# Optimization experiments

Measured on AMD Instinct MI355X. Metric: run time of the kernel, lower is better.

## Reference

```python
import jax, jax.numpy as jnp
import numpy as np


def setup_inputs() -> dict:
    key = jax.random.key(0)
    ks = jax.random.split(key, 8)
    b, cin, cout, h, w, t, ssize = 4, 128, 128, 64, 64, 16, 512
    return {
        "x": jax.random.normal(ks[0], (b, cin, h, w, t), jnp.float32),
        "style": jax.random.normal(ks[1], (b, ssize), jnp.float32),
        "noise": jax.random.normal(ks[2], (b, 1, h, w, t), jnp.float32),
        # learned params
        "weight": jax.random.normal(ks[3], (cout, cin, 3, 3, 1), jnp.float32),
        "style_w": jax.random.normal(ks[4], (cin, ssize), jnp.float32) * 0.02,
        "style_b": jax.random.normal(ks[5], (cin,), jnp.float32) * 0.02,
        "noise_param": jax.random.normal(ks[6], (cout, 1, 1, 1), jnp.float32) * 0.1,
        "bias_param": jax.random.normal(ks[7], (cout, 1, 1, 1), jnp.float32) * 0.1,
    }


def reference(x, style, noise, weight, style_w, style_b, noise_param, bias_param):
    # style modulation scale per (batch, in-channel)
    s = style @ style_w.T + style_b                         # [b, cin]
    # Demodulation factor per (b, out). Mathematically identical to building
    # per-sample weights W[o,i,k]*s[b,i] and demodulating, but computed as a
    # tiny contraction instead of materializing [b,out,in,k,k,1] weights.
    sig_inv = jax.lax.rsqrt(
        jnp.einsum('oihwt,bi->bo', weight**2, s**2) + 1e-8)  # [b, cout]
    # Since conv is linear in its input, scaling input channels by s and the
    # output channels by sig_inv equals the grouped per-sample conv.
    x_mod = x * s[:, :, None, None, None]                   # [b, cin, h, w, t]
    y = jax.lax.conv_general_dilated(
        x_mod, weight, window_strides=(1, 1, 1), padding='SAME',
        dimension_numbers=('NCDHW', 'OIDHW', 'NCDHW'))      # [b, cout, h, w, t]
    y = y * sig_inv[:, :, None, None, None]
    # noise_param/bias_param are [cout,1,1,1]; broadcast over (h,w,t)
    return y + noise_param * noise + bias_param
```

## Files before the change

### kernel.cpp

```cpp
#include <hip/hip_runtime.h>
#include <hip/hip_bf16.h>
#include <stdint.h>

typedef __bf16 bf16;
typedef bf16 bf16x8 __attribute__((ext_vector_type(8)));
typedef float f32x4 __attribute__((ext_vector_type(4)));
typedef float f32x16 __attribute__((ext_vector_type(16)));


__global__ void k_style(const float* __restrict__ style, const float* __restrict__ sw,
                        const float* __restrict__ sbias, float* __restrict__ s_out) {
    int gw = (blockIdx.x * blockDim.x + threadIdx.x) >> 6;
    int lane = threadIdx.x & 63;
    if (gw >= 512) return;
    int b = gw >> 7, c = gw & 127;
    const float* st = style + b * 512;
    const float* wr = sw + c * 512;
    float a = 0.f;
#pragma unroll
    for (int j = 0; j < 8; ++j) a += st[lane + 64 * j] * wr[lane + 64 * j];
    for (int off = 32; off > 0; off >>= 1) a += __shfl_down(a, off, 64);
    if (lane == 0) s_out[gw] = a + sbias[c];
}

__global__ void k_sig(const float* __restrict__ weight, const float* __restrict__ s,
                      float* __restrict__ sig) {
    int gw = (blockIdx.x * blockDim.x + threadIdx.x) >> 6;
    int lane = threadIdx.x & 63;
    if (gw >= 512) return;
    int b = gw >> 7, o = gw & 127;
    float a = 0.f;
#pragma unroll
    for (int j = 0; j < 2; ++j) {
        int i = lane + 64 * j;
        const float* wr = weight + ((size_t)o * 128 + i) * 9;
        float wsq = 0.f;
#pragma unroll
        for (int t = 0; t < 9; ++t) wsq += wr[t] * wr[t];
        float sv = s[b * 128 + i];
        a += wsq * sv * sv;
    }
    for (int off = 32; off > 0; off >>= 1) a += __shfl_down(a, off, 64);
    if (lane == 0) sig[gw] = rsqrtf(a + 1e-8f);
}

__global__ void k_wt(const float* __restrict__ weight, const float* __restrict__ s,
                     bf16* __restrict__ wt) {
    int i = blockIdx.x * 256 + threadIdx.x;
    if (i >= 589824) return;
    int j = i & 7;
    int co = (i >> 3) & 127;
    int g = (i >> 10) & 1;
    int tap = (i >> 11) % 9;
    int cb = (i >> 11) / 9;
    int chunk = cb & 7, b = cb >> 3;
    int ci = chunk * 16 + g * 8 + j;
    wt[i] = (bf16)(weight[((size_t)co * 128 + ci) * 9 + tap] * s[b * 128 + ci]);
}

__global__ __launch_bounds__(256, 2) void conv_main(
    const float* __restrict__ x, const bf16* __restrict__ wt,
    const float* __restrict__ sig_inv, const float* __restrict__ npar,
    const float* __restrict__ bpar, const float* __restrict__ noise,
    float* __restrict__ out) {
    __shared__ bf16 Xl[2][1728 * 8];

    const int tid = threadIdx.x;
    const int lane = tid & 63;
    const int l31 = lane & 31, lhi = lane >> 5;
    const int wm = (tid >> 6) & 1;
    const int wn = tid >> 7;
    const int w0 = blockIdx.x * 16;
    const int h = blockIdx.y;
    const int b = blockIdx.z;
    const size_t bHW = (size_t)b * 65536;

    auto stage = [&](int chunk, bf16* buf) {
        const bf16 zz = (bf16)0.f;
        const bf16x8 vz = {zz, zz, zz, zz, zz, zz, zz, zz};
#pragma unroll
        for (int it = 0; it < 7; ++it) {
            int u = it * 256 + tid;
            if (u < 1728) {
                int dh = u / 576;
                int rem = u - dh * 576;
                int g = rem / 288;
                int e = rem - g * 288;
                int ha = h - 1 + dh;
                int wa = w0 - 1 + (e >> 4);
                bool ok = ((unsigned)ha < 64u) & ((unsigned)wa < 64u);
                int E = (ha * 64 + wa) * 16 + (e & 15);
                int Ec = ok ? E : 0;
                const float* xp =
                    x + (((size_t)(b * 128 + chunk * 16 + g * 8)) << 16) + Ec;
                bf16x8 v;
#pragma unroll
                for (int j = 0; j < 8; ++j) v[j] = (bf16)xp[(size_t)j << 16];
                v = ok ? v : vz;
                *(bf16x8*)&buf[u * 8] = v;
            }
        }
    };

    f32x16 acc[2][4] = {};

    const size_t ebase = bHW + (size_t)h * 1024 + w0 * 16 + wn * 128;
    float ns[4];
#pragma unroll
    for (int nf = 0; nf < 4; ++nf) ns[nf] = noise[ebase + nf * 32 + l31];

    stage(0, Xl[0]);

    for (int chunk = 0; chunk < 8; ++chunk) {
        __syncthreads();
        if (chunk < 7) stage(chunk + 1, Xl[(chunk + 1) & 1]);
        const bf16* Xb = Xl[chunk & 1];
        const bf16* wb = wt + (size_t)b * 147456;

#pragma unroll
        for (int tap = 0; tap < 9; ++tap) {
            const int dh = tap / 3, dw = tap % 3;
            const bf16* wg = wb +
                ((size_t)((chunk * 9 + tap) * 2 + lhi) * 128 + wm * 64 + l31) * 8;
            bf16x8 a0 = *(const bf16x8*)&wg[0];
            bf16x8 a1 = *(const bf16x8*)&wg[32 * 8];
            const bf16* xb = &Xb[((dh * 2 + lhi) * 288 + dw * 16 + wn * 128 + l31) * 8];
            bf16x8 b0 = *(const bf16x8*)&xb[0];
            bf16x8 b1 = *(const bf16x8*)&xb[32 * 8];
            bf16x8 b2 = *(const bf16x8*)&xb[64 * 8];
            bf16x8 b3 = *(const bf16x8*)&xb[96 * 8];
            acc[0][0] = __builtin_amdgcn_mfma_f32_32x32x16_bf16(a0, b0, acc[0][0], 0, 0, 0);
            acc[0][1] = __builtin_amdgcn_mfma_f32_32x32x16_bf16(a0, b1, acc[0][1], 0, 0, 0);
            acc[0][2] = __builtin_amdgcn_mfma_f32_32x32x16_bf16(a0, b2, acc[0][2], 0, 0, 0);
            acc[0][3] = __builtin_amdgcn_mfma_f32_32x32x16_bf16(a0, b3, acc[0][3], 0, 0, 0);
            acc[1][0] = __builtin_amdgcn_mfma_f32_32x32x16_bf16(a1, b0, acc[1][0], 0, 0, 0);
            acc[1][1] = __builtin_amdgcn_mfma_f32_32x32x16_bf16(a1, b1, acc[1][1], 0, 0, 0);
            acc[1][2] = __builtin_amdgcn_mfma_f32_32x32x16_bf16(a1, b2, acc[1][2], 0, 0, 0);
            acc[1][3] = __builtin_amdgcn_mfma_f32_32x32x16_bf16(a1, b3, acc[1][3], 0, 0, 0);
        }
    }

#pragma unroll
    for (int fm = 0; fm < 2; ++fm) {
        int cob = wm * 64 + fm * 32 + 4 * lhi;
#pragma unroll
        for (int q = 0; q < 4; ++q) {
            int co4 = cob + 8 * q;
            f32x4 sg = *(const f32x4*)&sig_inv[b * 128 + co4];
            f32x4 np4 = *(const f32x4*)&npar[co4];
            f32x4 bp4 = *(const f32x4*)&bpar[co4];
#pragma unroll
            for (int r = 0; r < 4; ++r) {
                int co = co4 + r;
                float* orow = out + ((size_t)(b * 128 + co) * 64 + h) * 1024 +
                              w0 * 16 + wn * 128;
#pragma unroll
                for (int nf = 0; nf < 4; ++nf) {
                    float v = acc[fm][nf][q * 4 + r];
                    orow[nf * 32 + l31] = v * sg[r] + np4[r] * ns[nf] + bp4[r];
                }
            }
        }
    }
}

__global__ void k_naive(const float* __restrict__ x, const float* __restrict__ weight,
                        const float* __restrict__ s, const float* __restrict__ sig,
                        const float* __restrict__ npar, const float* __restrict__ bpar,
                        const float* __restrict__ noise, float* __restrict__ out) {
    size_t o = (size_t)blockIdx.x * 256 + threadIdx.x;
    int t = o & 15, w = (o >> 4) & 63, h = (o >> 10) & 63;
    int co = (o >> 16) & 127, b = (int)(o >> 23);
    float a = 0.f;
    for (int ci = 0; ci < 128; ++ci) {
        const float* xr = x + (size_t)(b * 128 + ci) * 65536;
        const float* wr = weight + ((size_t)co * 128 + ci) * 9;
        float p = 0.f;
#pragma unroll
        for (int kh = 0; kh < 3; ++kh) {
            int ha = h + kh - 1;
            if ((unsigned)ha >= 64u) continue;
#pragma unroll
            for (int kw = 0; kw < 3; ++kw) {
                int wa = w + kw - 1;
                if ((unsigned)wa >= 64u) continue;
                p += xr[(ha * 64 + wa) * 16 + t] * wr[kh * 3 + kw];
            }
        }
        a += p * s[b * 128 + ci];
    }
    int E = b * 65536 + (h * 64 + w) * 16 + t;
    out[o] = a * sig[b * 128 + co] + npar[co] * noise[E] + bpar[co];
}

extern "C" void kernel_launch(void* const* d_in, const int* in_sizes, int n_in,
                              void* d_out, int out_size, void* d_ws, size_t ws_size,
                              hipStream_t stream) {
    const float* x      = (const float*)d_in[0];
    const float* style  = (const float*)d_in[1];
    const float* noise  = (const float*)d_in[2];
    const float* weight = (const float*)d_in[3];
    const float* sw     = (const float*)d_in[4];
    const float* sb     = (const float*)d_in[5];
    const float* npar   = (const float*)d_in[6];
    const float* bpar   = (const float*)d_in[7];
    float* out = (float*)d_out;

    float* s_buf   = (float*)d_ws;
    float* sig_buf = s_buf + 512;
    bf16*  wt      = (bf16*)((char*)d_ws + 8192);
    const size_t NEED = 8192 + 4 * 294912ull;

    k_style<<<dim3(128), dim3(256), 0, stream>>>(style, sw, sb, s_buf);
    k_sig<<<dim3(128), dim3(256), 0, stream>>>(weight, s_buf, sig_buf);
    if (ws_size >= NEED) {
        k_wt<<<dim3(2304), dim3(256), 0, stream>>>(weight, s_buf, wt);
        conv_main<<<dim3(4, 64, 4), dim3(256), 0, stream>>>(
            x, wt, sig_buf, npar, bpar, noise, out);
    } else {
        k_naive<<<dim3(131072), dim3(256), 0, stream>>>(
            x, weight, s_buf, sig_buf, npar, bpar, noise, out);
    }
}
```

Before: 129.9 us.

## Load conv input fragments directly from global into registers, drop LDS staging

Removes the double-buffered shared-memory staging of the input tile and has each wave load its bf16 B-fragments straight from global memory into registers, reusing nine fragments across the three horizontal taps of each kernel row. This eliminates LDS writes/reads and __syncthreads barriers. It also switches to a 1D grid with a swizzled block-to-tile mapping that groups blocks across XCDs. The trade-off is redundant global loads across waves (each wave loads overlapping halos, and the two wm waves load identical data) with no software pipelining to hide load latency, plus higher register pressure.

```diff
diff --git a/kernel.cpp b/kernel.cpp
--- a/kernel.cpp
+++ b/kernel.cpp
@@ -63,44 +63,23 @@
     const float* __restrict__ sig_inv, const float* __restrict__ npar,
     const float* __restrict__ bpar, const float* __restrict__ noise,
     float* __restrict__ out) {
-    __shared__ bf16 Xl[2][1728 * 8];
-
     const int tid = threadIdx.x;
     const int lane = tid & 63;
     const int l31 = lane & 31, lhi = lane >> 5;
     const int wm = (tid >> 6) & 1;
     const int wn = tid >> 7;
-    const int w0 = blockIdx.x * 16;
-    const int h = blockIdx.y;
-    const int b = blockIdx.z;
+
+    const int hw = blockIdx.x;
+    const int logical = (hw & 7) * 128 + (hw >> 3);
+    const int w0 = (logical & 3) * 16;
+    const int h = (logical >> 2) & 63;
+    const int b = logical >> 8;
+
     const size_t bHW = (size_t)b * 65536;
-
-    auto stage = [&](int chunk, bf16* buf) {
-        const bf16 zz = (bf16)0.f;
-        const bf16x8 vz = {zz, zz, zz, zz, zz, zz, zz, zz};
-#pragma unroll
-        for (int it = 0; it < 7; ++it) {
-            int u = it * 256 + tid;
-            if (u < 1728) {
-                int dh = u / 576;
-                int rem = u - dh * 576;
-                int g = rem / 288;
-                int e = rem - g * 288;
-                int ha = h - 1 + dh;
-                int wa = w0 - 1 + (e >> 4);
-                bool ok = ((unsigned)ha < 64u) & ((unsigned)wa < 64u);
-                int E = (ha * 64 + wa) * 16 + (e & 15);
-                int Ec = ok ? E : 0;
-                const float* xp =
-                    x + (((size_t)(b * 128 + chunk * 16 + g * 8)) << 16) + Ec;
-                bf16x8 v;
-#pragma unroll
-                for (int j = 0; j < 8; ++j) v[j] = (bf16)xp[(size_t)j << 16];
-                v = ok ? v : vz;
-                *(bf16x8*)&buf[u * 8] = v;
-            }
-        }
-    };
+    const bf16* wb = wt + (size_t)b * 147456;
+
+    const bf16 zz = (bf16)0.f;
+    const bf16x8 vz = {zz, zz, zz, zz, zz, zz, zz, zz};
 
     f32x16 acc[2][4] = {};
 
@@ -109,34 +88,45 @@
 #pragma unroll
     for (int nf = 0; nf < 4; ++nf) ns[nf] = noise[ebase + nf * 32 + l31];
 
-    stage(0, Xl[0]);
-
-    for (int chunk = 0; chunk < 8; ++chunk) {
-        __syncthreads();
-        if (chunk < 7) stage(chunk + 1, Xl[(chunk + 1) & 1]);
-        const bf16* Xb = Xl[chunk & 1];
-        const bf16* wb = wt + (size_t)b * 147456;
-
-#pragma unroll
-        for (int tap = 0; tap < 9; ++tap) {
-            const int dh = tap / 3, dw = tap % 3;
-            const bf16* wg = wb +
-                ((size_t)((chunk * 9 + tap) * 2 + lhi) * 128 + wm * 64 + l31) * 8;
-            bf16x8 a0 = *(const bf16x8*)&wg[0];
-            bf16x8 a1 = *(const bf16x8*)&wg[32 * 8];
-            const bf16* xb = &Xb[((dh * 2 + lhi) * 288 + dw * 16 + wn * 128 + l31) * 8];
-            bf16x8 b0 = *(const bf16x8*)&xb[0];
-            bf16x8 b1 = *(const bf16x8*)&xb[32 * 8];
-            bf16x8 b2 = *(const bf16x8*)&xb[64 * 8];
-            bf16x8 b3 = *(const bf16x8*)&xb[96 * 8];
-            acc[0][0] = __builtin_amdgcn_mfma_f32_32x32x16_bf16(a0, b0, acc[0][0], 0, 0, 0);
-            acc[0][1] = __builtin_amdgcn_mfma_f32_32x32x16_bf16(a0, b1, acc[0][1], 0, 0, 0);
-            acc[0][2] = __builtin_amdgcn_mfma_f32_32x32x16_bf16(a0, b2, acc[0][2], 0, 0, 0);
-            acc[0][3] = __builtin_amdgcn_mfma_f32_32x32x16_bf16(a0, b3, acc[0][3], 0, 0, 0);
-            acc[1][0] = __builtin_amdgcn_mfma_f32_32x32x16_bf16(a1, b0, acc[1][0], 0, 0, 0);
-            acc[1][1] = __builtin_amdgcn_mfma_f32_32x32x16_bf16(a1, b1, acc[1][1], 0, 0, 0);
-            acc[1][2] = __builtin_amdgcn_mfma_f32_32x32x16_bf16(a1, b2, acc[1][2], 0, 0, 0);
-            acc[1][3] = __builtin_amdgcn_mfma_f32_32x32x16_bf16(a1, b3, acc[1][3], 0, 0, 0);
+    for (int c = 0; c < 8; ++c) {
+        const float* xc = x + (((size_t)(b * 128 + c * 16 + lhi * 8)) << 16);
+#pragma unroll
+        for (int dh = 0; dh < 3; ++dh) {
+            const int ha = h - 1 + dh;
+            const bool okh = (unsigned)ha < 64u;
+            const int Erow = ha * 1024 + (w0 - 1) * 16;
+
+            bf16x8 bf[9];
+#pragma unroll
+            for (int k = 0; k < 9; ++k) {
+                const int eoff = (k < 5) ? 32 * k : 16 + 32 * (k - 5);
+                const int e = wn * 128 + eoff + l31;
+                const int wa = w0 - 1 + (e >> 4);
+                const bool ok = okh & ((unsigned)wa < 64u);
+                const int Ec = ok ? (Erow + e) : 0;
+                bf16x8 v;
+#pragma unroll
+                for (int j = 0; j < 8; ++j)
+                    v[j] = (bf16)xc[((size_t)j << 16) + Ec];
+                bf[k] = ok ? v : vz;
+            }
+
+#pragma unroll
+            for (int dw = 0; dw < 3; ++dw) {
+                const bf16* wg = wb +
+                    ((size_t)((c * 9 + dh * 3 + dw) * 2 + lhi) * 128 + wm * 64 + l31) * 8;
+                bf16x8 a0 = *(const bf16x8*)&wg[0];
+                bf16x8 a1 = *(const bf16x8*)&wg[32 * 8];
+                const int i0 = (dw == 0) ? 0 : (dw == 1) ? 5 : 1;
+                acc[0][0] = __builtin_amdgcn_mfma_f32_32x32x16_bf16(a0, bf[i0 + 0], acc[0][0], 0, 0, 0);
+                acc[0][1] = __builtin_amdgcn_mfma_f32_32x32x16_bf16(a0, bf[i0 + 1], acc[0][1], 0, 0, 0);
+                acc[0][2] = __builtin_amdgcn_mfma_f32_32x32x16_bf16(a0, bf[i0 + 2], acc[0][2], 0, 0, 0);
+                acc[0][3] = __builtin_amdgcn_mfma_f32_32x32x16_bf16(a0, bf[i0 + 3], acc[0][3], 0, 0, 0);
+                acc[1][0] = __builtin_amdgcn_mfma_f32_32x32x16_bf16(a1, bf[i0 + 0], acc[1][0], 0, 0, 0);
+                acc[1][1] = __builtin_amdgcn_mfma_f32_32x32x16_bf16(a1, bf[i0 + 1], acc[1][1], 0, 0, 0);
+                acc[1][2] = __builtin_amdgcn_mfma_f32_32x32x16_bf16(a1, bf[i0 + 2], acc[1][2], 0, 0, 0);
+                acc[1][3] = __builtin_amdgcn_mfma_f32_32x32x16_bf16(a1, bf[i0 + 3], acc[1][3], 0, 0, 0);
+            }
         }
     }
 
@@ -215,7 +205,7 @@
     k_sig<<<dim3(128), dim3(256), 0, stream>>>(weight, s_buf, sig_buf);
     if (ws_size >= NEED) {
         k_wt<<<dim3(2304), dim3(256), 0, stream>>>(weight, s_buf, wt);
-        conv_main<<<dim3(4, 64, 4), dim3(256), 0, stream>>>(
+        conv_main<<<dim3(1024), dim3(256), 0, stream>>>(
             x, wt, sig_buf, npar, bpar, noise, out);
     } else {
         k_naive<<<dim3(131072), dim3(256), 0, stream>>>(
```

Measured after the change: 215.1 us. +65.5%, slower.
